# Performance work log

Hardware: AMD Instinct MI355X
Metric: run time of the kernel (lower is better)

The kernel has to match this reference:

```python
import jax, jax.numpy as jnp
import numpy as np

K = 20
BN_EPS = 1e-5


def setup_inputs() -> dict:
    key = jax.random.key(0)
    ks = jax.random.split(key, 8)
    B, N, C = 4, 8192, 128
    x = jax.random.normal(ks[0], (B, C, N), dtype=jnp.float32)
    xyz = jax.random.normal(ks[1], (B, N, 3), dtype=jnp.float32)
    # Conv1d(C+3 -> C, kernel_size=1): weight [C, C+3], bias [C]
    w1 = jax.random.normal(ks[2], (C, C + 3), dtype=jnp.float32) * 0.05
    b1 = jax.random.normal(ks[3], (C,), dtype=jnp.float32) * 0.05
    gamma = jnp.ones((C,), dtype=jnp.float32)
    beta = jnp.zeros((C,), dtype=jnp.float32)
    # Conv1d(C -> C, kernel_size=1)
    w2 = jax.random.normal(ks[4], (C, C), dtype=jnp.float32) * 0.05
    b2 = jax.random.normal(ks[5], (C,), dtype=jnp.float32) * 0.05
    return {"x": x, "xyz": xyz, "w1": w1, "b1": b1, "gamma": gamma,
            "beta": beta, "w2": w2, "b2": b2}


def _compute_normals(xyz):
    # xyz: [B, N, 3]
    sq = jnp.sum(xyz * xyz, axis=-1)                      # [B, N]
    dist = (-2.0 * jnp.einsum('bnc,bmc->bnm', xyz, xyz)
            + sq[:, :, None] + sq[:, None, :])            # [B, N, N]
    _, idx = jax.lax.top_k(-dist, K)                      # smallest-k -> [B, N, k]
    neighbors = jax.vmap(lambda pts, ix: pts[ix])(xyz, idx)  # [B, N, k, 3]
    nb = neighbors - xyz[:, :, None, :]                   # centered
    cov = jnp.einsum('bnkc,bnkd->bncd', nb, nb)           # [B, N, 3, 3]
    _, eigvecs = jnp.linalg.eigh(cov)                     # ascending eigenvalues
    return eigvecs[..., :, 0]                             # normal = smallest-eig vector, [B, N, 3]


def reference(x, xyz, w1, b1, gamma, beta, w2, b2):
    normals = _compute_normals(xyz)                       # [B, N, 3]
    geo = jnp.concatenate([x, jnp.transpose(normals, (0, 2, 1))], axis=1)  # [B, C+3, N]
    h = jnp.einsum('oc,bcn->bon', w1, geo) + b1[None, :, None]
    # BatchNorm1d (training mode, biased variance over (B, N))
    mean = jnp.mean(h, axis=(0, 2), keepdims=True)
    var = jnp.mean((h - mean) ** 2, axis=(0, 2), keepdims=True)
    h = gamma[None, :, None] * (h - mean) * jax.lax.rsqrt(var + BN_EPS) + beta[None, :, None]
    h = jax.nn.relu(h)
    out = jnp.einsum('oc,bcn->bon', w2, h) + b2[None, :, None]
    return out
```

## Files before the change

### kernel.cpp

```cpp
#include <hip/hip_runtime.h>
#include <math.h>

#define N_PTS 8192
#define BATCH 4
#define CH 128
#define KNN 20
#define CAP 112
#define STQ 114
#define POOL 256


__device__ __forceinline__ float slapy2f(float x, float y) {
#pragma clang fp contract(off)
  float ax = fabsf(x), ay = fabsf(y);
  float w = fmaxf(ax, ay), z = fminf(ax, ay);
  if (z == 0.0f) return w;
  float t = z / w;
  return w * sqrtf(1.0f + t * t);
}

__device__ __forceinline__ void slartgf(float f, float g, float* cs, float* sn, float* r) {
#pragma clang fp contract(off)
  if (g == 0.0f) { *cs = 1.0f; *sn = 0.0f; *r = f; }
  else if (f == 0.0f) { *cs = 0.0f; *sn = copysignf(1.0f, g); *r = fabsf(g); }
  else {
    float f1 = fabsf(f);
    float d = sqrtf(f * f + g * g);
    *cs = f1 / d;
    *r = copysignf(d, f);
    *sn = g / (*r);
  }
}

__device__ void slaev2f(float a, float b, float c, float* rt1, float* rt2,
                        float* cs1, float* sn1) {
#pragma clang fp contract(off)
  float sm = a + c, df = a - c, adf = fabsf(df);
  float tb = b + b, ab = fabsf(tb);
  float acmx, acmn;
  if (fabsf(a) > fabsf(c)) { acmx = a; acmn = c; } else { acmx = c; acmn = a; }
  float rt;
  if (adf > ab)      { float q = ab / adf;  rt = adf * sqrtf(1.0f + q * q); }
  else if (adf < ab) { float q = adf / ab;  rt = ab * sqrtf(1.0f + q * q); }
  else               rt = ab * sqrtf(2.0f);
  int sgn1;
  if (sm < 0.0f)      { *rt1 = 0.5f * (sm - rt); sgn1 = -1; *rt2 = (acmx / *rt1) * acmn - (b / *rt1) * b; }
  else if (sm > 0.0f) { *rt1 = 0.5f * (sm + rt); sgn1 = 1;  *rt2 = (acmx / *rt1) * acmn - (b / *rt1) * b; }
  else                { *rt1 = 0.5f * rt; *rt2 = -0.5f * rt; sgn1 = 1; }
  float cs; int sgn2;
  if (df >= 0.0f) { cs = df + rt; sgn2 = 1; } else { cs = df - rt; sgn2 = -1; }
  float acs = fabsf(cs);
  if (acs > ab) {
    float ct = -tb / cs;
    *sn1 = 1.0f / sqrtf(1.0f + ct * ct);
    *cs1 = ct * (*sn1);
  } else {
    if (ab == 0.0f) { *cs1 = 1.0f; *sn1 = 0.0f; }
    else {
      float tn = -cs / tb;
      *cs1 = 1.0f / sqrtf(1.0f + tn * tn);
      *sn1 = tn * (*cs1);
    }
  }
  if (sgn1 == sgn2) { float tn = *cs1; *cs1 = -(*sn1); *sn1 = tn; }
}

__device__ void eigh3_smallest(float a00, float a10, float a20,
                               float a11, float a21, float a22, float evec[3]) {
#pragma clang fp contract(off)
  float d[3], e[2], tau = 0.0f, v2 = 0.0f;
  d[0] = a00;
  {
    float xnorm = sqrtf(a20 * a20);
    if (xnorm == 0.0f) {
      tau = 0.0f; v2 = 0.0f;
      e[0] = a10; d[1] = a11; e[1] = a21; d[2] = a22;
    } else {
      float alpha = a10;
      float beta = -copysignf(slapy2f(alpha, xnorm), alpha);
      tau = (beta - alpha) / beta;
      float invs = 1.0f / (alpha - beta);
      v2 = a20 * invs;
      e[0] = beta;
      float y0 = tau * a11;
      float y1 = tau * a21;
      y0 = y0 + tau * (a21 * v2);
      y1 = y1 + (tau * v2) * a22;
      float dot = y0 + y1 * v2;
      float al = (-0.5f * tau) * dot;
      float w0 = y0 + al;
      float w1 = y1 + al * v2;
      a11 = (a11 - w0) - w0;
      a21 = (a21 - v2 * w0) - w1;
      a22 = (a22 - v2 * w1) - w1 * v2;
      d[1] = a11; e[1] = a21; d[2] = a22;
    }
  }

  float z[3][3] = {{1.0f,0.0f,0.0f},{0.0f,1.0f,0.0f},{0.0f,0.0f,1.0f}};
  const float eps = 5.9604644775390625e-08f;
  const float eps2 = 3.5527136788005009e-15f;
  const float safmin = 1.1754943508222875e-38f;
  int nmaxit = 90, jtot = 0;
  int l1 = 0;
  int l, m, lend, lsv, lendsv;
  float p, g, r, c, s, f, b_, rt1, rt2, tst;
  float wc[2], wsn[2];

outer_loop:
  if (l1 > 2) goto sorting;
  if (l1 > 0) e[l1 - 1] = 0.0f;
  {
    int mm;
    for (mm = l1; mm <= 1; ++mm) {
      tst = fabsf(e[mm]);
      if (tst == 0.0f) break;
      if (tst <= (sqrtf(fabsf(d[mm])) * sqrtf(fabsf(d[mm + 1]))) * eps) { e[mm] = 0.0f; break; }
    }
    m = (mm > 1) ? 2 : mm;
  }
  l = l1; lsv = l; lend = m; lendsv = lend; l1 = m + 1;
  if (lend == l) goto outer_loop;
  {
    float an = 0.0f;
    for (int i2 = l; i2 <= lend; ++i2) an = fmaxf(an, fabsf(d[i2]));
    for (int i2 = l; i2 < lend; ++i2) an = fmaxf(an, fabsf(e[i2]));
    if (an == 0.0f) goto outer_loop;
  }
  if (fabsf(d[lend]) < fabsf(d[l])) { lend = lsv; l = lendsv; }

  if (lend > l) {
ql40:
    if (l != lend) {
      for (m = l; m <= lend - 1; ++m) {
        tst = e[m] * e[m];
        if (tst <= (eps2 * fabsf(d[m])) * fabsf(d[m + 1]) + safmin) goto ql60;
      }
    }
    m = lend;
ql60:
    if (m < lend) e[m] = 0.0f;
    p = d[l];
    if (m == l) goto ql80;
    if (m == l + 1) {
      slaev2f(d[l], e[l], d[l + 1], &rt1, &rt2, &c, &s);
      for (int i2 = 0; i2 < 3; ++i2) {
        float temp = z[i2][l + 1];
        z[i2][l + 1] = c * temp - s * z[i2][l];
        z[i2][l]     = s * temp + c * z[i2][l];
      }
      d[l] = rt1; d[l + 1] = rt2; e[l] = 0.0f;
      l += 2;
      if (l <= lend) goto ql40;
      goto done140;
    }
    if (jtot == nmaxit) goto done140;
    jtot++;
    g = (d[l + 1] - p) / (2.0f * e[l]);
    r = slapy2f(g, 1.0f);
    g = d[m] - p + e[l] / (g + copysignf(r, g));
    s = 1.0f; c = 1.0f; p = 0.0f;
    for (int i2 = m - 1; i2 >= l; --i2) {
      f = s * e[i2]; b_ = c * e[i2];
      slartgf(g, f, &c, &s, &r);
      if (i2 != m - 1) e[i2 + 1] = r;
      g = d[i2 + 1] - p;
      r = (d[i2] - g) * s + 2.0f * c * b_;
      p = s * r;
      d[i2 + 1] = g + p;
      g = c * r - b_;
      wc[i2] = c; wsn[i2] = -s;
    }
    for (int j = m - 1; j >= l; --j) {
      float ct = wc[j], st = wsn[j];
      for (int i2 = 0; i2 < 3; ++i2) {
        float temp = z[i2][j + 1];
        z[i2][j + 1] = ct * temp - st * z[i2][j];
        z[i2][j]     = st * temp + ct * z[i2][j];
      }
    }
    d[l] -= p;
    e[l] = g;
    goto ql40;
ql80:
    d[l] = p;
    l += 1;
    if (l <= lend) goto ql40;
    goto done140;
  } else {
qr90:
    if (l != lend) {
      for (m = l; m >= lend + 1; --m) {
        tst = e[m - 1] * e[m - 1];
        if (tst <= (eps2 * fabsf(d[m])) * fabsf(d[m - 1]) + safmin) goto qr110;
      }
    }
    m = lend;
qr110:
    if (m > lend) e[m - 1] = 0.0f;
    p = d[l];
    if (m == l) goto qr130;
    if (m == l - 1) {
      slaev2f(d[l - 1], e[l - 1], d[l], &rt1, &rt2, &c, &s);
      for (int i2 = 0; i2 < 3; ++i2) {
        float temp = z[i2][l];
        z[i2][l]     = c * temp - s * z[i2][l - 1];
        z[i2][l - 1] = s * temp + c * z[i2][l - 1];
      }
      d[l - 1] = rt1; d[l] = rt2; e[l - 1] = 0.0f;
      l -= 2;
      if (l >= lend) goto qr90;
      goto done140;
    }
    if (jtot == nmaxit) goto done140;
    jtot++;
    g = (d[l - 1] - p) / (2.0f * e[l - 1]);
    r = slapy2f(g, 1.0f);
    g = d[m] - p + e[l - 1] / (g + copysignf(r, g));
    s = 1.0f; c = 1.0f; p = 0.0f;
    for (int i2 = m; i2 <= l - 1; ++i2) {
      f = s * e[i2]; b_ = c * e[i2];
      slartgf(g, f, &c, &s, &r);
      if (i2 != m) e[i2 - 1] = r;
      g = d[i2] - p;
      r = (d[i2 + 1] - g) * s + 2.0f * c * b_;
      p = s * r;
      d[i2] = g + p;
      g = c * r - b_;
      wc[i2] = c; wsn[i2] = s;
    }
    for (int j = m; j <= l - 1; ++j) {
      float ct = wc[j], st = wsn[j];
      for (int i2 = 0; i2 < 3; ++i2) {
        float temp = z[i2][j + 1];
        z[i2][j + 1] = ct * temp - st * z[i2][j];
        z[i2][j]     = st * temp + ct * z[i2][j];
      }
    }
    d[l] -= p;
    e[l - 1] = g;
    goto qr90;
qr130:
    d[l] = p;
    l -= 1;
    if (l >= lend) goto qr90;
    goto done140;
  }
done140:
  if (jtot < nmaxit) goto outer_loop;
sorting:
  for (int ii = 1; ii <= 2; ++ii) {
    int i_ = ii - 1, k = i_;
    p = d[i_];
    for (int j = ii; j <= 2; ++j) if (d[j] < p) { k = j; p = d[j]; }
    if (k != i_) {
      d[k] = d[i_]; d[i_] = p;
      for (int i2 = 0; i2 < 3; ++i2) { float tz = z[i2][i_]; z[i2][i_] = z[i2][k]; z[i2][k] = tz; }
    }
  }
  {
    float z10 = z[1][0], z20 = z[2][0];
    float sum = z10 + v2 * z20;
    evec[0] = z[0][0];
    evec[1] = z10 - tau * sum;
    evec[2] = z20 - tau * sum * v2;
  }
}

__global__ __launch_bounds__(256) void prep_kernel(const float* __restrict__ xyz,
                                                   const float* __restrict__ w1,
                                                   const float* __restrict__ w2,
                                                   float4* __restrict__ xyz4,
                                                   float* __restrict__ w1t,
                                                   float* __restrict__ w2t,
                                                   float* __restrict__ stats) {
  int idx = blockIdx.x * 256 + threadIdx.x;
  if (idx < BATCH * N_PTS) {
    float x = xyz[idx * 3], y = xyz[idx * 3 + 1], zz = xyz[idx * 3 + 2];
    float sq = fmaf(zz, zz, fmaf(y, y, x * x));
    xyz4[idx] = make_float4(x, y, zz, -0.5f * sq);
  }
  if (idx < 132 * CH) {
    int cc = idx >> 7, o = idx & 127;
    w1t[idx] = (cc < 131) ? w1[o * 131 + cc] : 0.0f;
  }
  if (idx < CH * CH) {
    int cc = idx >> 7, o = idx & 127;
    w2t[idx] = w2[o * CH + cc];
  }
  if (idx < 256) stats[idx] = 0.0f;
}

__device__ __forceinline__ float qdist2(const float4 qv, const float4 cv) {
  float dot = fmaf(qv.x, cv.x, fmaf(qv.y, cv.y, qv.z * cv.z));
  return fmaf(-2.0f, dot, (-2.0f * qv.w) + (-2.0f * cv.w));
}

__device__ __forceinline__ unsigned int distbits(float dist) {
  unsigned int du = __float_as_uint(dist);
  return (du & 0x80000000u) ? ~du : (du | 0x80000000u);
}

__global__ __launch_bounds__(1024, 8) void knn_select_kernel(const float4* __restrict__ xyz4,
                                                             unsigned short* __restrict__ nidx) {
  __shared__ unsigned int lst_d[64 * STQ];
  __shared__ unsigned short lst_i[64 * STQ];
  __shared__ float2 bnd[16 * 64];
  __shared__ unsigned long long pool[POOL];
  __shared__ unsigned int qcnt[64];
  __shared__ unsigned int qflag[64];
  __shared__ unsigned int qover[64];
  __shared__ unsigned int pool_cnt;

  const int t = threadIdx.x;
  const int w = t >> 6, l = t & 63;
  const int batch = blockIdx.x >> 7;
  const int q0 = (blockIdx.x & 127) << 6;
  const float4* __restrict__ xb = xyz4 + batch * N_PTS;
  const float4 qv = xb[q0 + l];
  const float qw = -2.0f * qv.w;

  if (t < 64) { qcnt[t] = 0; qflag[t] = 0; qover[t] = 0; }
  if (t == 0) pool_cnt = 0;

  const int base = __builtin_amdgcn_readfirstlane(w * 512);

#define KF(cv) fmaf(qv.x, (cv).x, fmaf(qv.y, (cv).y, fmaf(qv.z, (cv).z, (cv).w)))

  float a0 = -INFINITY, a1 = -INFINITY;
  {
    float4 pA0 = xb[base + 0], pA1 = xb[base + 1], pA2 = xb[base + 2], pA3 = xb[base + 3];
    float4 pB0 = xb[base + 4], pB1 = xb[base + 5], pB2 = xb[base + 6], pB3 = xb[base + 7];
#define TOP2(kk) { float tt = fminf(a0, kk); a0 = fmaxf(a0, kk); a1 = fmaxf(a1, tt); }
    for (int i = 0; i < 512; i += 8) {
      float k0 = KF(pA0); pA0 = xb[base + i + 8];
      float k1 = KF(pA1); pA1 = xb[base + i + 9];
      float k2 = KF(pA2); pA2 = xb[base + i + 10];
      float k3 = KF(pA3); pA3 = xb[base + i + 11];
      TOP2(k0) TOP2(k1) TOP2(k2) TOP2(k3)
      k0 = KF(pB0); pB0 = xb[base + i + 12];
      k1 = KF(pB1); pB1 = xb[base + i + 13];
      k2 = KF(pB2); pB2 = xb[base + i + 14];
      k3 = KF(pB3); pB3 = xb[base + i + 15];
      TOP2(k0) TOP2(k1) TOP2(k2) TOP2(k3)
    }
#undef TOP2
  }
  bnd[w * 64 + l] = make_float2(a0, a1);
  __syncthreads();

  float kmin = INFINITY;
#pragma unroll
  for (int g = 0; g < 8; ++g) {
    float2 pa = bnd[(2 * g) * 64 + l];
    float2 pb = bnd[(2 * g + 1) * 64 + l];
    float third = fmaxf(fminf(pa.y, pb.x), fminf(pa.x, pb.y));
    kmin = fminf(kmin, third);
  }
  float Tq = fmaf(-2.0f, kmin, qw);
  Tq = Tq + (fabsf(Tq) * 2e-5f + 1e-3f);
  const float thK = 0.5f * (qw - Tq) - 1e-3f;

  {
    float4 pA0 = xb[base + 0], pA1 = xb[base + 1], pA2 = xb[base + 2], pA3 = xb[base + 3];
    float4 pB0 = xb[base + 4], pB1 = xb[base + 5], pB2 = xb[base + 6], pB3 = xb[base + 7];
#define COLLECT(cv, idx_) {                                                     \
      float k = KF(cv);                                                         \
      if (k >= thK) {                                                           \
        float dot = fmaf(qv.x, (cv).x, fmaf(qv.y, (cv).y, qv.z * (cv).z));      \
        float dist = fmaf(-2.0f, dot, qw + (-2.0f * (cv).w));                   \
        if (dist <= Tq) {                                                       \
          unsigned int db = distbits(dist);                                     \
          unsigned int pos = atomicAdd(&qcnt[l], 1u);                           \
          if (pos < CAP) {                                                      \
            lst_d[l * STQ + pos] = db;                                          \
            lst_i[l * STQ + pos] = (unsigned short)(idx_);                      \
          } else {                                                              \
            unsigned long long key = ((unsigned long long)db << 32)             \
                                   | ((unsigned int)l << 16) | (unsigned int)(idx_); \
            unsigned int pp = atomicAdd(&pool_cnt, 1u);                         \
            if (pp < POOL) { pool[pp] = key; qflag[l] = 1u; }                   \
            else qover[l] = 1u;                                                 \
          }                                                                     \
        }                                                                       \
      }                                                                         \
    }
    for (int i = 0; i < 512; i += 8) {
      float4 cA0 = pA0; pA0 = xb[base + i + 8];
      float4 cA1 = pA1; pA1 = xb[base + i + 9];
      float4 cA2 = pA2; pA2 = xb[base + i + 10];
      float4 cA3 = pA3; pA3 = xb[base + i + 11];
      COLLECT(cA0, base + i)     COLLECT(cA1, base + i + 1)
      COLLECT(cA2, base + i + 2) COLLECT(cA3, base + i + 3)
      float4 cB0 = pB0; pB0 = xb[base + i + 12];
      float4 cB1 = pB1; pB1 = xb[base + i + 13];
      float4 cB2 = pB2; pB2 = xb[base + i + 14];
      float4 cB3 = pB3; pB3 = xb[base + i + 15];
      COLLECT(cB0, base + i + 4) COLLECT(cB1, base + i + 5)
      COLLECT(cB2, base + i + 6) COLLECT(cB3, base + i + 7)
    }
#undef COLLECT
  }
#undef KF
  __syncthreads();

  const int qg = t >> 4, sub = t & 15;
  unsigned int n = qcnt[qg]; if (n > CAP) n = CAP;
  const unsigned int pcnt = (qflag[qg] && !qover[qg]) ? min(pool_cnt, (unsigned int)POOL) : 0u;
  unsigned short* oq = nidx + ((size_t)(batch * N_PTS + q0 + qg)) * KNN;

  if (qover[qg]) {
    if (sub == 0) {
      unsigned long long best[KNN];
#pragma unroll
      for (int j = 0; j < KNN; ++j) best[j] = ~0ULL;
      const float4 qv2 = xb[q0 + qg];
      for (int m = 0; m < N_PTS; ++m) {
        float dist = qdist2(qv2, xb[m]);
        unsigned long long p = ((unsigned long long)distbits(dist) << 32) | (unsigned int)m;
        if (p < best[KNN - 1]) {
          int j = KNN - 1;
          while (j > 0 && best[j - 1] > p) { best[j] = best[j - 1]; --j; }
          best[j] = p;
        }
      }
      for (int j = 0; j < KNN; ++j) oq[j] = (unsigned short)(best[j] & 0xffffu);
    }
  } else {
    for (int r = 0; r < KNN; ++r) {
      unsigned long long best = ~0ULL; int bslot = 0;
      for (unsigned int s = sub; s < n; s += 16) {
        unsigned long long v = ((unsigned long long)lst_d[qg * STQ + s] << 16)
                             | (unsigned long long)lst_i[qg * STQ + s];
        if (v < best) { best = v; bslot = (int)s; }
      }
      for (unsigned int s = sub; s < pcnt; s += 16) {
        unsigned long long v = pool[s];
        if ((unsigned int)((v >> 16) & 0xffffu) == (unsigned int)qg) {
          unsigned long long pv = ((v >> 32) << 16) | (v & 0xffffULL);
          if (pv < best) { best = pv; bslot = 0x10000 | (int)s; }
        }
      }
#pragma unroll
      for (int mm = 1; mm < 16; mm <<= 1) {
        unsigned long long ob = __shfl_xor(best, mm, 64);
        int obs = __shfl_xor(bslot, mm, 64);
        if (ob < best) { best = ob; bslot = obs; }
      }
      int s = bslot & 0xffff;
      if ((s & 15) == sub) {
        if (bslot & 0x10000) pool[s] = ~0ULL;
        else lst_d[qg * STQ + s] = 0xFFFFFFFFu;
      }
      if (sub == 0) oq[r] = (unsigned short)(best & 0xffffu);
    }
  }
}

__global__ __launch_bounds__(64) void normals_kernel(const float4* __restrict__ xyz4,
                                                     const unsigned short* __restrict__ nidx,
                                                     float4* __restrict__ nrm4) {
  int gid = blockIdx.x * 64 + threadIdx.x;
  int batch = gid >> 13, q = gid & (N_PTS - 1);
  const float4* __restrict__ xb = xyz4 + batch * N_PTS;
  const float4 qv = xb[q];
  const unsigned short* iq = nidx + (size_t)gid * KNN;
  float c00, c01, c02, c11, c12, c22;
  {
#pragma clang fp contract(off)
    c00 = 0.f; c01 = 0.f; c02 = 0.f; c11 = 0.f; c12 = 0.f; c22 = 0.f;
    for (int j = 0; j < KNN; ++j) {
      float4 pv = xb[iq[j]];
      float dx = pv.x - qv.x, dy = pv.y - qv.y, dz = pv.z - qv.z;
      c00 = c00 + dx * dx; c01 = c01 + dx * dy; c02 = c02 + dx * dz;
      c11 = c11 + dy * dy; c12 = c12 + dy * dz; c22 = c22 + dz * dz;
    }
  }
  float ev[3];
  eigh3_smallest(c00, c01, c02, c11, c12, c22, ev);
  nrm4[gid] = make_float4(ev[0], ev[1], ev[2], 0.0f);
}

__global__ __launch_bounds__(256) void gemm1_stats_kernel(const float* __restrict__ x,
                                                          const float4* __restrict__ nrm4,
                                                          const float* __restrict__ w1t,
                                                          const float* __restrict__ b1,
                                                          float* __restrict__ sums,
                                                          float* __restrict__ sumsq) {
  __shared__ float lds[64 * 134];
  const int t = threadIdx.x;
  const int b = blockIdx.x >> 7;
  const int n0 = (blockIdx.x & 127) << 6;
  for (int idx = t; idx < CH * 64; idx += 256) {
    int cc = idx >> 6, nl = idx & 63;
    lds[nl * 134 + cc] = x[((size_t)(b * CH + cc)) * N_PTS + n0 + nl];
  }
  if (t < 64) {
    float4 nv = nrm4[b * N_PTS + n0 + t];
    lds[t * 134 + 128] = nv.x; lds[t * 134 + 129] = nv.y;
    lds[t * 134 + 130] = nv.z; lds[t * 134 + 131] = 0.0f;
  }
  __syncthreads();

  const int og = __builtin_amdgcn_readfirstlane(t >> 6);
  const int nl = t & 63;
  float acc[32];
#pragma unroll
  for (int k = 0; k < 32; ++k) acc[k] = b1[og * 32 + k];
  for (int c2 = 0; c2 < 66; ++c2) {
    float2 xv = *(const float2*)&lds[nl * 134 + 2 * c2];
    const float* wr0 = w1t + (2 * c2) * CH + og * 32;
    const float* wr1 = wr0 + CH;
#pragma unroll
    for (int k = 0; k < 32; ++k) acc[k] = fmaf(wr0[k], xv.x, acc[k]);
#pragma unroll
    for (int k = 0; k < 32; ++k) acc[k] = fmaf(wr1[k], xv.y, acc[k]);
  }
  __syncthreads();
#pragma unroll
  for (int k2 = 0; k2 < 16; ++k2)
    *(float2*)&lds[nl * 134 + og * 32 + 2 * k2] = make_float2(acc[2 * k2], acc[2 * k2 + 1]);
  __syncthreads();
  {
    int cc = t & 127, hf = t >> 7;
    float sm = 0.f, sq = 0.f;
    for (int rr = hf * 32; rr < hf * 32 + 32; ++rr) {
      float v = lds[rr * 134 + cc];
      sm += v; sq = fmaf(v, v, sq);
    }
    atomicAdd(&sums[cc], sm);
    atomicAdd(&sumsq[cc], sq);
  }
}

__global__ void bn_finalize_kernel(const float* __restrict__ sums, const float* __restrict__ sumsq,
                                   const float* __restrict__ gamma, const float* __restrict__ beta,
                                   float* __restrict__ scale, float* __restrict__ shift) {
  int c = threadIdx.x;
  if (c < CH) {
    const double cnt = (double)(BATCH * N_PTS);
    double mean = (double)sums[c] / cnt;
    double var = (double)sumsq[c] / cnt - mean * mean;
    double inv = 1.0 / sqrt(var + 1e-5);
    double sc = (double)gamma[c] * inv;
    scale[c] = (float)sc;
    shift[c] = (float)((double)beta[c] - mean * sc);
  }
}

__global__ __launch_bounds__(256) void fused_out_kernel(const float* __restrict__ x,
                                                        const float4* __restrict__ nrm4,
                                                        const float* __restrict__ w1t,
                                                        const float* __restrict__ b1,
                                                        const float* __restrict__ w2t,
                                                        const float* __restrict__ b2,
                                                        const float* __restrict__ scale,
                                                        const float* __restrict__ shift,
                                                        float* __restrict__ out) {
  __shared__ float lds[64 * 134];
  const int t = threadIdx.x;
  const int b = blockIdx.x >> 7;
  const int n0 = (blockIdx.x & 127) << 6;
  for (int idx = t; idx < CH * 64; idx += 256) {
    int cc = idx >> 6, nl = idx & 63;
    lds[nl * 134 + cc] = x[((size_t)(b * CH + cc)) * N_PTS + n0 + nl];
  }
  if (t < 64) {
    float4 nv = nrm4[b * N_PTS + n0 + t];
    lds[t * 134 + 128] = nv.x; lds[t * 134 + 129] = nv.y;
    lds[t * 134 + 130] = nv.z; lds[t * 134 + 131] = 0.0f;
  }
  __syncthreads();

  const int og = __builtin_amdgcn_readfirstlane(t >> 6);
  const int nl = t & 63;
  float acc[32];
#pragma unroll
  for (int k = 0; k < 32; ++k) acc[k] = b1[og * 32 + k];
  for (int c2 = 0; c2 < 66; ++c2) {
    float2 xv = *(const float2*)&lds[nl * 134 + 2 * c2];
    const float* wr0 = w1t + (2 * c2) * CH + og * 32;
    const float* wr1 = wr0 + CH;
#pragma unroll
    for (int k = 0; k < 32; ++k) acc[k] = fmaf(wr0[k], xv.x, acc[k]);
#pragma unroll
    for (int k = 0; k < 32; ++k) acc[k] = fmaf(wr1[k], xv.y, acc[k]);
  }
#pragma unroll
  for (int k = 0; k < 32; ++k) {
    float sc = scale[og * 32 + k], sh = shift[og * 32 + k];
    acc[k] = fmaxf(fmaf(acc[k], sc, sh), 0.0f);
  }
  __syncthreads();
#pragma unroll
  for (int k2 = 0; k2 < 16; ++k2)
    *(float2*)&lds[nl * 134 + og * 32 + 2 * k2] = make_float2(acc[2 * k2], acc[2 * k2 + 1]);
  __syncthreads();

  float acc2[32];
#pragma unroll
  for (int k = 0; k < 32; ++k) acc2[k] = b2[og * 32 + k];
  for (int c2 = 0; c2 < 64; ++c2) {
    float2 hv = *(const float2*)&lds[nl * 134 + 2 * c2];
    const float* wr0 = w2t + (2 * c2) * CH + og * 32;
    const float* wr1 = wr0 + CH;
#pragma unroll
    for (int k = 0; k < 32; ++k) acc2[k] = fmaf(wr0[k], hv.x, acc2[k]);
#pragma unroll
    for (int k = 0; k < 32; ++k) acc2[k] = fmaf(wr1[k], hv.y, acc2[k]);
  }
#pragma unroll
  for (int k = 0; k < 32; ++k) {
    int o = og * 32 + k;
    out[((size_t)(b * CH + o)) * N_PTS + n0 + nl] = acc2[k];
  }
}

extern "C" void kernel_launch(void* const* d_in, const int* in_sizes, int n_in,
                              void* d_out, int out_size, void* d_ws, size_t ws_size,
                              hipStream_t stream) {
  const float* x     = (const float*)d_in[0];
  const float* xyz   = (const float*)d_in[1];
  const float* w1    = (const float*)d_in[2];
  const float* b1    = (const float*)d_in[3];
  const float* gamma = (const float*)d_in[4];
  const float* beta  = (const float*)d_in[5];
  const float* w2    = (const float*)d_in[6];
  const float* b2    = (const float*)d_in[7];
  float* out = (float*)d_out;

  float* W = (float*)d_ws;
  float4* xyz4 = (float4*)W;
  float4* nrm4 = (float4*)(W + 131072);
  float* w1t   = W + 262144;
  float* w2t   = W + 279040;
  float* stats = W + 295424;
  float* scale = W + 295680;
  float* shift = W + 295808;
  unsigned short* nidx = (unsigned short*)(W + 295936);

  prep_kernel<<<128, 256, 0, stream>>>(xyz, w1, w2, xyz4, w1t, w2t, stats);
  knn_select_kernel<<<BATCH * N_PTS / 64, 1024, 0, stream>>>(xyz4, nidx);
  normals_kernel<<<BATCH * N_PTS / 64, 64, 0, stream>>>(xyz4, nidx, nrm4);
  gemm1_stats_kernel<<<BATCH * N_PTS / 64, 256, 0, stream>>>(x, nrm4, w1t, b1, stats, stats + 128);
  bn_finalize_kernel<<<1, 128, 0, stream>>>(stats, stats + 128, gamma, beta, scale, shift);
  fused_out_kernel<<<BATCH * N_PTS / 64, 256, 0, stream>>>(x, nrm4, w1t, b1, w2t, b2, scale, shift, out);
}
```

Measured before the change: 359.1 us.

## Store first GEMM output and fuse BN finalize into second GEMM kernel

The first GEMM kernel now writes its pre-norm activations h to workspace, so the output kernel no longer recomputes the first GEMM. The new output kernel reads h, computes the BN scale and shift per block (replacing the separate finalize launch), applies BN and ReLU in LDS, then runs the second GEMM. This trades the GEMM1 recompute for an extra 16 MB write and read of h. It falls back to the old path when the workspace is too small.

New measurement: 351.5 us. 1.02x faster.

```diff
diff --git a/kernel.cpp b/kernel.cpp
--- a/kernel.cpp
+++ b/kernel.cpp
@@ -486,7 +486,8 @@
                                                           const float* __restrict__ w1t,
                                                           const float* __restrict__ b1,
                                                           float* __restrict__ sums,
-                                                          float* __restrict__ sumsq) {
+                                                          float* __restrict__ sumsq,
+                                                          float* __restrict__ h) {
   __shared__ float lds[64 * 134];
   const int t = threadIdx.x;
   const int b = blockIdx.x >> 7;
@@ -515,6 +516,13 @@
     for (int k = 0; k < 32; ++k) acc[k] = fmaf(wr0[k], xv.x, acc[k]);
 #pragma unroll
     for (int k = 0; k < 32; ++k) acc[k] = fmaf(wr1[k], xv.y, acc[k]);
+  }
+  if (h != nullptr) {
+#pragma unroll
+    for (int k = 0; k < 32; ++k) {
+      int o = og * 32 + k;
+      h[((size_t)(b * CH + o)) * N_PTS + n0 + nl] = acc[k];
+    }
   }
   __syncthreads();
 #pragma unroll
@@ -545,6 +553,62 @@
     double sc = (double)gamma[c] * inv;
     scale[c] = (float)sc;
     shift[c] = (float)((double)beta[c] - mean * sc);
+  }
+}
+
+__global__ __launch_bounds__(256) void bn_out_kernel(const float* __restrict__ h,
+                                                     const float* __restrict__ w2t,
+                                                     const float* __restrict__ b2,
+                                                     const float* __restrict__ sums,
+                                                     const float* __restrict__ sumsq,
+                                                     const float* __restrict__ gamma,
+                                                     const float* __restrict__ beta,
+                                                     float* __restrict__ out) {
+  __shared__ float lds[64 * 134];
+  __shared__ float s_scale[CH];
+  __shared__ float s_shift[CH];
+  const int t = threadIdx.x;
+  const int b = blockIdx.x >> 7;
+  const int n0 = (blockIdx.x & 127) << 6;
+  if (t < CH) {
+    const double cnt = (double)(BATCH * N_PTS);
+    double mean = (double)sums[t] / cnt;
+    double var = (double)sumsq[t] / cnt - mean * mean;
+    double inv = 1.0 / sqrt(var + 1e-5);
+    double sc = (double)gamma[t] * inv;
+    s_scale[t] = (float)sc;
+    s_shift[t] = (float)((double)beta[t] - mean * sc);
+  }
+  for (int idx = t; idx < CH * 64; idx += 256) {
+    int cc = idx >> 6, nl = idx & 63;
+    lds[nl * 134 + cc] = h[((size_t)(b * CH + cc)) * N_PTS + n0 + nl];
+  }
+  __syncthreads();
+  for (int idx = t; idx < CH * 64; idx += 256) {
+    int cc = idx >> 6, nl = idx & 63;
+    float v = lds[nl * 134 + cc];
+    lds[nl * 134 + cc] = fmaxf(fmaf(v, s_scale[cc], s_shift[cc]), 0.0f);
+  }
+  __syncthreads();
+
+  const int og = __builtin_amdgcn_readfirstlane(t >> 6);
+  const int nl = t & 63;
+  float acc2[32];
+#pragma unroll
+  for (int k = 0; k < 32; ++k) acc2[k] = b2[og * 32 + k];
+  for (int c2 = 0; c2 < 64; ++c2) {
+    float2 hv = *(const float2*)&lds[nl * 134 + 2 * c2];
+    const float* wr0 = w2t + (2 * c2) * CH + og * 32;
+    const float* wr1 = wr0 + CH;
+#pragma unroll
+    for (int k = 0; k < 32; ++k) acc2[k] = fmaf(wr0[k], hv.x, acc2[k]);
+#pragma unroll
+    for (int k = 0; k < 32; ++k) acc2[k] = fmaf(wr1[k], hv.y, acc2[k]);
+  }
+#pragma unroll
+  for (int k = 0; k < 32; ++k) {
+    int o = og * 32 + k;
+    out[((size_t)(b * CH + o)) * N_PTS + n0 + nl] = acc2[k];
   }
 }
 
@@ -638,11 +702,21 @@
   float* scale = W + 295680;
   float* shift = W + 295808;
   unsigned short* nidx = (unsigned short*)(W + 295936);
+  float* h     = W + 624640;
+
+  const size_t need = (size_t)(624640 + (size_t)BATCH * CH * N_PTS) * 4;
+  const bool use_h = (ws_size >= need);
 
   prep_kernel<<<128, 256, 0, stream>>>(xyz, w1, w2, xyz4, w1t, w2t, stats);
   knn_select_kernel<<<BATCH * N_PTS / 64, 1024, 0, stream>>>(xyz4, nidx);
   normals_kernel<<<BATCH * N_PTS / 64, 64, 0, stream>>>(xyz4, nidx, nrm4);
-  gemm1_stats_kernel<<<BATCH * N_PTS / 64, 256, 0, stream>>>(x, nrm4, w1t, b1, stats, stats + 128);
-  bn_finalize_kernel<<<1, 128, 0, stream>>>(stats, stats + 128, gamma, beta, scale, shift);
-  fused_out_kernel<<<BATCH * N_PTS / 64, 256, 0, stream>>>(x, nrm4, w1t, b1, w2t, b2, scale, shift, out);
-}
+  gemm1_stats_kernel<<<BATCH * N_PTS / 64, 256, 0, stream>>>(x, nrm4, w1t, b1, stats, stats + 128,
+                                                             use_h ? h : nullptr);
+  if (use_h) {
+    bn_out_kernel<<<BATCH * N_PTS / 64, 256, 0, stream>>>(h, w2t, b2, stats, stats + 128,
+                                                          gamma, beta, out);
+  } else {
+    bn_finalize_kernel<<<1, 128, 0, stream>>>(stats, stats + 128, gamma, beta, scale, shift);
+    fused_out_kernel<<<BATCH * N_PTS / 64, 256, 0, stream>>>(x, nrm4, w1t, b1, w2t, b2, scale, shift, out);
+  }
+}
```
